# Optimization experiments

Measured on AMD Instinct MI355X. Metric: run time of the kernel, lower is better.

## Reference

```python
import jax, jax.numpy as jnp
import numpy as np

NEG_SLOPE = 0.2

def setup_inputs() -> dict:
    key = jax.random.key(0)
    ks = jax.random.split(key, 6)
    N, E, D_in, D_out = 100000, 1000000, 128, 64
    x = jax.random.normal(ks[0], (N, D_in), dtype=jnp.float32)
    W = jax.random.normal(ks[1], (D_in, D_out), dtype=jnp.float32) / np.sqrt(D_in)
    att_src = jax.random.normal(ks[2], (D_out,), dtype=jnp.float32) / np.sqrt(D_out)
    att_dst = jax.random.normal(ks[3], (D_out,), dtype=jnp.float32) / np.sqrt(D_out)
    bias = jax.random.normal(ks[4], (D_out,), dtype=jnp.float32) * 0.01
    edge_index = jax.random.randint(ks[5], (2, E), 0, N, dtype=jnp.int64)
    return {"x": x, "W": W, "att_src": att_src, "att_dst": att_dst, "bias": bias, "edge_index": edge_index}

def reference(x, W, att_src, att_dst, bias, edge_index):
    N = x.shape[0]
    # GATConv with add_self_loops=True (PyG default)
    loops = jnp.arange(N, dtype=edge_index.dtype)
    src = jnp.concatenate([edge_index[0], loops])  # message source j
    dst = jnp.concatenate([edge_index[1], loops])  # aggregation target i
    h = x @ W                                      # [N, D_out]
    a_src = h @ att_src                            # [N]
    a_dst = h @ att_dst                            # [N]
    e = a_src[src] + a_dst[dst]                    # [E+N]
    e = jnp.where(e > 0, e, NEG_SLOPE * e)         # leaky_relu(0.2)
    # segment softmax over incoming edges of each dst node
    m = jax.ops.segment_max(e, dst, num_segments=N)        # every node has a self loop
    ex = jnp.exp(e - m[dst])
    denom = jax.ops.segment_sum(ex, dst, num_segments=N)
    alpha = ex / denom[dst]                        # [E+N]
    out = jax.ops.segment_sum(h[src] * alpha[:, None], dst, num_segments=N)
    out = out + bias
    return jax.nn.elu(out)
```

## Files before the change

kernel.cpp:

```cpp
#include <hip/hip_runtime.h>
#include <math.h>

#define NEG_SLOPE 0.2f

__device__ inline ushort f2bf(float f) {
    unsigned u = __float_as_uint(f);
    u += 0x7fffu + ((u >> 16) & 1u);
    return (ushort)(u >> 16);
}

__global__ __launch_bounds__(256) void k_gemm_att(
    const float* __restrict__ x, const float* __restrict__ W,
    const float* __restrict__ att_src, const float* __restrict__ att_dst,
    ushort* __restrict__ hb, float* __restrict__ a_src, float* __restrict__ a_dst,
    int N)
{
    __shared__ float xs[64 * 128];
    __shared__ float Ws[128 * 64];
    const int t = threadIdx.x;

    #pragma unroll
    for (int i = 0; i < 8; ++i) {
        int idx = t + i * 256;
        ((float4*)Ws)[idx] = ((const float4*)W)[idx];
    }
    const int row0 = blockIdx.x * 64;
    #pragma unroll
    for (int i = 0; i < 8; ++i) {
        int idx = t + i * 256;
        int r = idx >> 5;
        int c = (idx & 31) << 2;
        int cs = c ^ (((r >> 2) & 3) << 3);
        float4 v = make_float4(0.f, 0.f, 0.f, 0.f);
        if (row0 + r < N) v = *(const float4*)(x + (size_t)(row0 + r) * 128 + c);
        *(float4*)&xs[r * 128 + cs] = v;
    }
    __syncthreads();

    const int tr  = (t >> 4) << 2;
    const int tc  = (t & 15) << 2;
    const int swz = ((t >> 4) & 3) << 3;

    float acc[4][4] = {};
    #pragma unroll 8
    for (int k = 0; k < 128; k += 2) {
        float4 w0 = *(const float4*)&Ws[k * 64 + tc];
        float4 w1 = *(const float4*)&Ws[(k + 1) * 64 + tc];
        #pragma unroll
        for (int i = 0; i < 4; ++i) {
            float2 xv = *(const float2*)&xs[(tr + i) * 128 + (k ^ swz)];
            acc[i][0] = fmaf(xv.x, w0.x, fmaf(xv.y, w1.x, acc[i][0]));
            acc[i][1] = fmaf(xv.x, w0.y, fmaf(xv.y, w1.y, acc[i][1]));
            acc[i][2] = fmaf(xv.x, w0.z, fmaf(xv.y, w1.z, acc[i][2]));
            acc[i][3] = fmaf(xv.x, w0.w, fmaf(xv.y, w1.w, acc[i][3]));
        }
    }

    const float4 as4 = *(const float4*)(att_src + tc);
    const float4 ad4 = *(const float4*)(att_dst + tc);
    #pragma unroll
    for (int i = 0; i < 4; ++i) {
        int row = row0 + tr + i;
        float ps = acc[i][0]*as4.x + acc[i][1]*as4.y + acc[i][2]*as4.z + acc[i][3]*as4.w;
        float pd = acc[i][0]*ad4.x + acc[i][1]*ad4.y + acc[i][2]*ad4.z + acc[i][3]*ad4.w;
        #pragma unroll
        for (int o = 8; o >= 1; o >>= 1) {
            ps += __shfl_xor(ps, o);
            pd += __shfl_xor(pd, o);
        }
        if (row < N) {
            ushort4 hv;
            hv.x = f2bf(acc[i][0]); hv.y = f2bf(acc[i][1]);
            hv.z = f2bf(acc[i][2]); hv.w = f2bf(acc[i][3]);
            *(ushort4*)&hb[(size_t)row * 64 + tc] = hv;
            if ((t & 15) == 0) { a_src[row] = ps; a_dst[row] = pd; }
        }
    }
}

__global__ __launch_bounds__(256) void k_hist(
    const int* __restrict__ dst_idx, int* __restrict__ deg, int E, int M)
{
    long m = (long)blockIdx.x * blockDim.x + threadIdx.x;
    if (m >= M) return;
    int d = (m < E) ? dst_idx[m] : (int)(m - E);
    atomicAdd(deg + d, 1);
}

__global__ __launch_bounds__(256) void k_scan_part(
    const int* __restrict__ deg, int* __restrict__ partials, int N)
{
    __shared__ int red[4];
    const int base = blockIdx.x * 2048;
    int s = 0;
    #pragma unroll
    for (int i = 0; i < 8; ++i) {
        int idx = base + threadIdx.x + i * 256;
        if (idx < N) s += deg[idx];
    }
    #pragma unroll
    for (int o = 32; o >= 1; o >>= 1) s += __shfl_xor(s, o);
    if ((threadIdx.x & 63) == 0) red[threadIdx.x >> 6] = s;
    __syncthreads();
    if (threadIdx.x == 0)
        partials[blockIdx.x] = red[0] + red[1] + red[2] + red[3];
}

__global__ __launch_bounds__(256) void k_scan_tops(
    int* __restrict__ partials, int* __restrict__ off, int G, int N)
{
    __shared__ int sh[256];
    const int t = threadIdx.x;
    int v = (t < G) ? partials[t] : 0;
    sh[t] = v;
    __syncthreads();
    for (int d = 1; d < 256; d <<= 1) {
        int u = (t >= d) ? sh[t - d] : 0;
        __syncthreads();
        sh[t] += u;
        __syncthreads();
    }
    if (t < G) partials[t] = sh[t] - v;
    if (t == 255) off[N] = sh[255];
}

__global__ __launch_bounds__(256) void k_scan_down(
    const int* __restrict__ deg, const int* __restrict__ partials,
    int* __restrict__ off, int* __restrict__ woff, int N)
{
    __shared__ int tsum[256];
    const int t = threadIdx.x;
    const int base = blockIdx.x * 2048 + t * 8;
    int v[8];
    int s = 0;
    #pragma unroll
    for (int j = 0; j < 8; ++j) {
        int idx = base + j;
        v[j] = (idx < N) ? deg[idx] : 0;
        s += v[j];
    }
    tsum[t] = s;
    __syncthreads();
    for (int d = 1; d < 256; d <<= 1) {
        int u = (t >= d) ? tsum[t - d] : 0;
        __syncthreads();
        tsum[t] += u;
        __syncthreads();
    }
    int excl = partials[blockIdx.x] + (t ? tsum[t - 1] : 0);
    #pragma unroll
    for (int j = 0; j < 8; ++j) {
        int idx = base + j;
        if (idx < N) { off[idx] = excl; woff[idx] = excl; }
        excl += v[j];
    }
}

__global__ __launch_bounds__(256) void k_scatter(
    const int* __restrict__ src_idx, const int* __restrict__ dst_idx,
    const float* __restrict__ a_src, const float* __restrict__ a_dst,
    int* __restrict__ woff, int2* __restrict__ sorted, int E, int M)
{
    long m = (long)blockIdx.x * blockDim.x + threadIdx.x;
    if (m >= M) return;
    int s, d;
    if (m < E) { s = src_idx[m]; d = dst_idx[m]; }
    else       { s = d = (int)(m - E); }
    float e = a_src[s] + a_dst[d];
    e = e > 0.f ? e : NEG_SLOPE * e;
    float ex = __expf(e);
    int pos = atomicAdd(woff + d, 1);
    sorted[pos] = make_int2(s, __float_as_int(ex));
}

__global__ __launch_bounds__(256) void k_gather(
    const int2* __restrict__ sorted, const int* __restrict__ off,
    const ushort* __restrict__ hb, const float* __restrict__ bias,
    float* __restrict__ out, int N)
{
    const int lane = threadIdx.x & 63;
    const int d    = blockIdx.x * (blockDim.x >> 6) + (threadIdx.x >> 6);
    if (d >= N) return;
    const int beg = off[d], end = off[d + 1];
    const int g   = lane >> 3;
    const int sub = lane & 7;

    float acc[8] = {0.f,0.f,0.f,0.f,0.f,0.f,0.f,0.f};
    float dsum = 0.f;

    for (int base = beg; base < end; base += 8) {
        int j = base + g;
        int2 meta = (j < end) ? sorted[j] : make_int2(0, 0);
        float ex = __int_as_float(meta.y);
        dsum += (sub == 0) ? ex : 0.f;
        uint4 raw = *(const uint4*)(hb + (size_t)meta.x * 64 + sub * 8);
        acc[0] = fmaf(__uint_as_float(raw.x << 16),          ex, acc[0]);
        acc[1] = fmaf(__uint_as_float(raw.x & 0xffff0000u),  ex, acc[1]);
        acc[2] = fmaf(__uint_as_float(raw.y << 16),          ex, acc[2]);
        acc[3] = fmaf(__uint_as_float(raw.y & 0xffff0000u),  ex, acc[3]);
        acc[4] = fmaf(__uint_as_float(raw.z << 16),          ex, acc[4]);
        acc[5] = fmaf(__uint_as_float(raw.z & 0xffff0000u),  ex, acc[5]);
        acc[6] = fmaf(__uint_as_float(raw.w << 16),          ex, acc[6]);
        acc[7] = fmaf(__uint_as_float(raw.w & 0xffff0000u),  ex, acc[7]);
    }

    #pragma unroll
    for (int o = 8; o <= 32; o <<= 1)
        #pragma unroll
        for (int p = 0; p < 8; ++p) acc[p] += __shfl_xor(acc[p], o);
    #pragma unroll
    for (int o = 1; o <= 32; o <<= 1) dsum += __shfl_xor(dsum, o);

    float val = 0.f;
    #pragma unroll
    for (int p = 0; p < 8; ++p) {
        float v = __shfl(acc[p], g);
        if (sub == p) val = v;
    }

    float r = val / dsum + bias[lane];
    out[(size_t)d * 64 + lane] = r > 0.f ? r : expm1f(r);
}

extern "C" void kernel_launch(void* const* d_in, const int* in_sizes, int n_in,
                              void* d_out, int out_size, void* d_ws, size_t ws_size,
                              hipStream_t stream)
{
    const float* x       = (const float*)d_in[0];
    const float* W       = (const float*)d_in[1];
    const float* att_src = (const float*)d_in[2];
    const float* att_dst = (const float*)d_in[3];
    const float* bias    = (const float*)d_in[4];
    const int*   eidx    = (const int*)d_in[5];

    const int N = in_sizes[0] / 128;
    const int E = in_sizes[5] / 2;
    const int M = E + N;

    float* out = (float*)d_out;

    ushort* hb    = (ushort*)d_ws;
    float*  a_src = (float*)(hb + (size_t)N * 64);
    float*  a_dst = a_src + N;
    int*    deg   = (int*)(a_dst + N);
    int*    off   = deg + N;
    int*    woff  = off + N + 1;
    int*    parts = woff + N + 1;
    size_t  sofs  = (size_t)(parts + 256 - (int*)d_ws);
    sofs = (sofs + 1) & ~(size_t)1;
    int2*   sorted = (int2*)((int*)d_ws + sofs);

    const int G = (N + 2047) / 2048;

    hipMemsetAsync(deg, 0, (size_t)N * sizeof(int), stream);

    k_gemm_att<<<(N + 63) / 64, 256, 0, stream>>>(x, W, att_src, att_dst,
                                                  hb, a_src, a_dst, N);
    k_hist<<<(M + 255) / 256, 256, 0, stream>>>(eidx + E, deg, E, M);
    k_scan_part<<<G, 256, 0, stream>>>(deg, parts, N);
    k_scan_tops<<<1, 256, 0, stream>>>(parts, off, G, N);
    k_scan_down<<<G, 256, 0, stream>>>(deg, parts, off, woff, N);
    k_scatter<<<(M + 255) / 256, 256, 0, stream>>>(eidx, eidx + E, a_src, a_dst,
                                                   woff, sorted, E, M);
    k_gather<<<(N + 3) / 4, 256, 0, stream>>>(sorted, off, hb, bias, out, N);
}
```

Before: 287.5 us.

## Merge histogram into GEMM launch and move edge-score computation into gather

```diff
diff --git a/kernel.cpp b/kernel.cpp
--- a/kernel.cpp
+++ b/kernel.cpp
@@ -9,22 +9,36 @@
     return (ushort)(u >> 16);
 }
 
-__global__ __launch_bounds__(256) void k_gemm_att(
+__global__ __launch_bounds__(256) void k_gemm_hist(
     const float* __restrict__ x, const float* __restrict__ W,
     const float* __restrict__ att_src, const float* __restrict__ att_dst,
     ushort* __restrict__ hb, float* __restrict__ a_src, float* __restrict__ a_dst,
-    int N)
+    const int* __restrict__ dst_idx, int* __restrict__ deg,
+    int N, int E, int M, int Gh)
 {
     __shared__ float xs[64 * 128];
     __shared__ float Ws[128 * 64];
     const int t = threadIdx.x;
 
+    if (blockIdx.x < Gh) {
+        long base = (long)blockIdx.x * 2048 + t;
+        #pragma unroll
+        for (int i = 0; i < 8; ++i) {
+            long m = base + i * 256;
+            if (m < M) {
+                int d = (m < E) ? dst_idx[m] : (int)(m - E);
+                atomicAdd(deg + d, 1);
+            }
+        }
+        return;
+    }
+
     #pragma unroll
     for (int i = 0; i < 8; ++i) {
         int idx = t + i * 256;
         ((float4*)Ws)[idx] = ((const float4*)W)[idx];
     }
-    const int row0 = blockIdx.x * 64;
+    const int row0 = (blockIdx.x - Gh) * 64;
     #pragma unroll
     for (int i = 0; i < 8; ++i) {
         int idx = t + i * 256;
@@ -78,15 +92,6 @@
     }
 }
 
-__global__ __launch_bounds__(256) void k_hist(
-    const int* __restrict__ dst_idx, int* __restrict__ deg, int E, int M)
-{
-    long m = (long)blockIdx.x * blockDim.x + threadIdx.x;
-    if (m >= M) return;
-    int d = (m < E) ? dst_idx[m] : (int)(m - E);
-    atomicAdd(deg + d, 1);
-}
-
 __global__ __launch_bounds__(256) void k_scan_part(
     const int* __restrict__ deg, int* __restrict__ partials, int N)
 {
@@ -158,23 +163,20 @@
 
 __global__ __launch_bounds__(256) void k_scatter(
     const int* __restrict__ src_idx, const int* __restrict__ dst_idx,
-    const float* __restrict__ a_src, const float* __restrict__ a_dst,
-    int* __restrict__ woff, int2* __restrict__ sorted, int E, int M)
+    int* __restrict__ woff, int* __restrict__ sorted, int E, int M)
 {
     long m = (long)blockIdx.x * blockDim.x + threadIdx.x;
     if (m >= M) return;
     int s, d;
     if (m < E) { s = src_idx[m]; d = dst_idx[m]; }
     else       { s = d = (int)(m - E); }
-    float e = a_src[s] + a_dst[d];
-    e = e > 0.f ? e : NEG_SLOPE * e;
-    float ex = __expf(e);
     int pos = atomicAdd(woff + d, 1);
-    sorted[pos] = make_int2(s, __float_as_int(ex));
+    sorted[pos] = s;
 }
 
 __global__ __launch_bounds__(256) void k_gather(
-    const int2* __restrict__ sorted, const int* __restrict__ off,
+    const int* __restrict__ srcs, const int* __restrict__ off,
+    const float* __restrict__ a_src, const float* __restrict__ a_dst,
     const ushort* __restrict__ hb, const float* __restrict__ bias,
     float* __restrict__ out, int N)
 {
@@ -184,16 +186,22 @@
     const int beg = off[d], end = off[d + 1];
     const int g   = lane >> 3;
     const int sub = lane & 7;
+    const float adst = a_dst[d];
 
     float acc[8] = {0.f,0.f,0.f,0.f,0.f,0.f,0.f,0.f};
     float dsum = 0.f;
 
     for (int base = beg; base < end; base += 8) {
         int j = base + g;
-        int2 meta = (j < end) ? sorted[j] : make_int2(0, 0);
-        float ex = __int_as_float(meta.y);
+        int src = 0; float ex = 0.f;
+        if (j < end) {
+            src = srcs[j];
+            float e = a_src[src] + adst;
+            e = e > 0.f ? e : NEG_SLOPE * e;
+            ex = __expf(e);
+        }
         dsum += (sub == 0) ? ex : 0.f;
-        uint4 raw = *(const uint4*)(hb + (size_t)meta.x * 64 + sub * 8);
+        uint4 raw = *(const uint4*)(hb + (size_t)src * 64 + sub * 8);
         acc[0] = fmaf(__uint_as_float(raw.x << 16),          ex, acc[0]);
         acc[1] = fmaf(__uint_as_float(raw.x & 0xffff0000u),  ex, acc[1]);
         acc[2] = fmaf(__uint_as_float(raw.y << 16),          ex, acc[2]);
@@ -246,21 +254,22 @@
     int*    off   = deg + N;
     int*    woff  = off + N + 1;
     int*    parts = woff + N + 1;
-    size_t  sofs  = (size_t)(parts + 256 - (int*)d_ws);
-    sofs = (sofs + 1) & ~(size_t)1;
-    int2*   sorted = (int2*)((int*)d_ws + sofs);
-
-    const int G = (N + 2047) / 2048;
+    int*    sorted = parts + 256;
+
+    const int G  = (N + 2047) / 2048;
+    const int Gh = (M + 2047) / 2048;
+    const int Gg = (N + 63) / 64;
 
     hipMemsetAsync(deg, 0, (size_t)N * sizeof(int), stream);
 
-    k_gemm_att<<<(N + 63) / 64, 256, 0, stream>>>(x, W, att_src, att_dst,
-                                                  hb, a_src, a_dst, N);
-    k_hist<<<(M + 255) / 256, 256, 0, stream>>>(eidx + E, deg, E, M);
+    k_gemm_hist<<<Gh + Gg, 256, 0, stream>>>(x, W, att_src, att_dst,
+                                             hb, a_src, a_dst,
+                                             eidx + E, deg, N, E, M, Gh);
     k_scan_part<<<G, 256, 0, stream>>>(deg, parts, N);
     k_scan_tops<<<1, 256, 0, stream>>>(parts, off, G, N);
     k_scan_down<<<G, 256, 0, stream>>>(deg, parts, off, woff, N);
-    k_scatter<<<(M + 255) / 256, 256, 0, stream>>>(eidx, eidx + E, a_src, a_dst,
+    k_scatter<<<(M + 255) / 256, 256, 0, stream>>>(eidx, eidx + E,
                                                    woff, sorted, E, M);
-    k_gather<<<(N + 3) / 4, 256, 0, stream>>>(sorted, off, hb, bias, out, N);
-}
+    k_gather<<<(N + 3) / 4, 256, 0, stream>>>(sorted, off, a_src, a_dst,
+                                              hb, bias, out, N);
+}
```

Measured after the change: 301.7 us. 4.9% more time.
